# Optimization experiments

Hardware: AMD Instinct MI355X
Metric: run time of the kernel (lower is better)

Reference implementation:

```python
import jax, jax.numpy as jnp
import numpy as np

B, T, C = 1, 2048, 1024
H = 16
HD = C // H
BLOCK = 2048
NEG = float('-inf')

def setup_inputs() -> dict:
    key = jax.random.key(0)
    ks = jax.random.split(key, 6)
    x = jax.random.normal(ks[0], (B, T, C), dtype=jnp.float32)
    cumulative_scores = jax.random.normal(ks[1], (B, T), dtype=jnp.float32) * 0.1
    padding_mask = jnp.ones((B, T), dtype=jnp.float32)
    token_index = jax.random.randint(ks[2], (B, T), 0, BLOCK).astype(jnp.int64)
    w_attn = jax.random.normal(ks[3], (C, 3 * C), dtype=jnp.float32) * (1.0 / np.sqrt(C))
    b_attn = jnp.zeros((3 * C,), dtype=jnp.float32)
    w_proj = jax.random.normal(ks[4], (C, C), dtype=jnp.float32) * (1.0 / np.sqrt(C))
    b_proj = jnp.zeros((C,), dtype=jnp.float32)
    return dict(x=x, cumulative_scores=cumulative_scores, padding_mask=padding_mask,
                token_index=token_index, w_attn=w_attn, b_attn=b_attn,
                w_proj=w_proj, b_proj=b_proj)

def _rotate_half(z):
    z1, z2 = z[..., : z.shape[-1] // 2], z[..., z.shape[-1] // 2 :]
    return jnp.concatenate((-z2, z1), axis=-1)

def reference(x, cumulative_scores, padding_mask, token_index, w_attn, b_attn, w_proj, b_proj):
    # fused QKV projection
    qkv = x @ w_attn + b_attn                      # (B,T,3C)
    q, k, v = jnp.split(qkv, 3, axis=2)
    q = q.reshape(B, T, H, HD).transpose(0, 2, 1, 3)  # (B,H,T,HD)
    k = k.reshape(B, T, H, HD).transpose(0, 2, 1, 3)
    v = v.reshape(B, T, H, HD).transpose(0, 2, 1, 3)

    # dynamic per-token RoPE positions: global token counts (original scatter
    # broadcasts indices over batch, so counts are global across all batches)
    cnt = jnp.zeros((BLOCK,), jnp.float32).at[token_index.reshape(-1)].add(1.0)
    per_tok = (1.0 / (cnt + 1e-10))[token_index]       # (B,T)
    partial = jnp.cumsum(per_tok, axis=-1)             # (B,T) fractional positions

    inv_freq = 1.0 / (10000.0 ** (jnp.arange(0, HD, 2, dtype=jnp.float32) / HD))
    freqs = partial[..., None] * inv_freq              # (B,T,HD/2)
    emb = jnp.concatenate((freqs, freqs), axis=-1)     # (B,T,HD)
    cos = jnp.cos(emb)[:, None]                        # (B,1,T,HD)
    sin = jnp.sin(emb)[:, None]
    q = q * cos + _rotate_half(q) * sin
    k = k * cos + _rotate_half(k) * sin

    # 'fork' plan: overwrite last channel
    q = q.at[..., -1].set(1.0)
    k = k.at[..., -1].set(jnp.broadcast_to(cumulative_scores[:, None, :], (B, H, T)))

    # additive causal + padding mask (B,T,T)
    causal = jnp.where(jnp.tril(jnp.ones((T, T), jnp.bool_)), 0.0, NEG)
    pm = jnp.take_along_axis(padding_mask, token_index, axis=1)     # (B,T)
    outer = pm[:, :, None] * pm[:, None, :]
    pad_add = jnp.where(outer.astype(jnp.bool_), 0.0, NEG)
    mask = causal[None, :, :] + pad_add                              # (B,T,T)

    # scale v by exp(cumulative_scores)
    v = v * jnp.exp(cumulative_scores)[:, None, :, None]

    scores = jnp.einsum('bhqd,bhkd->bhqk', q, k) / np.sqrt(HD) + mask[:, None]
    probs = jax.nn.softmax(scores, axis=-1)
    y = jnp.einsum('bhqk,bhkd->bhqd', probs, v)        # (B,H,T,HD)
    y = y.transpose(0, 2, 1, 3).reshape(B, T, C)
    return y @ w_proj + b_proj
```

## Files before the change

kernel.cpp:

```cpp
#include <hip/hip_runtime.h>
#include <math.h>

#define T 2048
#define C 1024
#define H 16
#define HD 64
#define N3 (3*C)
#define NBLOCK 2048

typedef __attribute__((ext_vector_type(8))) short bf16x8;
typedef __attribute__((ext_vector_type(4))) float f32x4;

#define MFMA16(a, b, c) __builtin_amdgcn_mfma_f32_16x16x32_bf16((a), (b), (c), 0, 0, 0)

__device__ inline short f2bf(float f) {
    unsigned u; __builtin_memcpy(&u, &f, 4);
    unsigned r = (u + 0x7fffu + ((u >> 16) & 1u)) >> 16;
    return (short)r;
}
__device__ inline float bf2f(short s) {
    unsigned u = ((unsigned)(unsigned short)s) << 16;
    float f; __builtin_memcpy(&f, &u, 4);
    return f;
}

__device__ inline void gload_lds16(const void* g, void* l) {
    __builtin_amdgcn_global_load_lds((const __attribute__((address_space(1))) unsigned int*)g,
                                     (__attribute__((address_space(3))) unsigned int*)l,
                                     16, 0, 0);
}

__global__ __launch_bounds__(256) void pre_kernel(const float* __restrict__ x,
                                                  const float* __restrict__ w_attn,
                                                  const float* __restrict__ w_proj,
                                                  const int* __restrict__ tok,
                                                  const float* __restrict__ padmask,
                                                  short* __restrict__ xb,
                                                  short* __restrict__ wabT,
                                                  short* __restrict__ wpbT,
                                                  float* __restrict__ partial,
                                                  float* __restrict__ pm_tok) {
    int bid = blockIdx.x;
    int tid = threadIdx.x;
    if (bid == 3072) {
        __shared__ float cntS[NBLOCK];
        __shared__ float sums[256];
        #pragma unroll
        for (int j = 0; j < 8; ++j) cntS[tid * 8 + j] = 0.0f;
        __syncthreads();
        int tk[8];
        #pragma unroll
        for (int j = 0; j < 8; ++j) {
            tk[j] = tok[tid * 8 + j];
            atomicAdd(&cntS[tk[j]], 1.0f);
        }
        __syncthreads();
        float vals[8];
        float s = 0.0f;
        #pragma unroll
        for (int j = 0; j < 8; ++j) {
            s += 1.0f / (cntS[tk[j]] + 1e-10f);
            vals[j] = s;
            pm_tok[tid * 8 + j] = padmask[tk[j]];
        }
        sums[tid] = s;
        __syncthreads();
        for (int off = 1; off < 256; off <<= 1) {
            float v = (tid >= off) ? sums[tid - off] : 0.0f;
            __syncthreads();
            sums[tid] += v;
            __syncthreads();
        }
        float offset = (tid > 0) ? sums[tid - 1] : 0.0f;
        #pragma unroll
        for (int j = 0; j < 8; ++j) partial[tid * 8 + j] = offset + vals[j];
        return;
    }
    if (bid < 2048) {
        int i = bid * 1024 + tid * 4;
        float4 v = *(const float4*)(x + i);
        short4 o;
        o.x = f2bf(v.x); o.y = f2bf(v.y); o.z = f2bf(v.z); o.w = f2bf(v.w);
        *(short4*)(xb + i) = o;
        return;
    }
    __shared__ float S[64][65];
    const float* in; short* out; int Kd, Nd, bx, by;
    if (bid < 2816) {
        int b = bid - 2048;
        bx = b % 48; by = b / 48;
        in = w_attn; out = wabT; Kd = C; Nd = N3;
    } else {
        int b = bid - 2816;
        bx = b % 16; by = b / 16;
        in = w_proj; out = wpbT; Kd = C; Nd = C;
    }
    int n0 = bx * 64, k0 = by * 64;
    #pragma unroll
    for (int i = 0; i < 16; ++i) {
        int lin = tid + i * 256;
        int r = lin >> 6, c = lin & 63;
        S[r][c] = in[(size_t)(k0 + r) * Nd + n0 + c];
    }
    __syncthreads();
    #pragma unroll
    for (int i = 0; i < 16; ++i) {
        int lin = tid + i * 256;
        int rn = lin >> 6, ck = lin & 63;
        out[(size_t)(n0 + rn) * Kd + k0 + ck] = f2bf(S[ck][rn]);
    }
}

template <int OUT_BF16, int BNF>
__global__ __launch_bounds__(256) void gemm_bt(const short* __restrict__ A,
                                               const short* __restrict__ Bt,
                                               const float* __restrict__ bias,
                                               void* __restrict__ Cout,
                                               int M, int N, int K) {
    constexpr int BN = BNF * 32;
    __shared__ alignas(16) short As[128 * 32];
    __shared__ alignas(16) short Bs[BN * 32];
    int tid = threadIdx.x;
    int m0 = blockIdx.y * 128, n0 = blockIdx.x * BN;
    int w = tid >> 6, l = tid & 63;
    int wm = (w >> 1) * 64, wn = (w & 1) * (BNF * 16);
    int lq = l & 15, g = l >> 4;
    int prow = l >> 2, pcol = (l & 3) * 8;
    f32x4 acc[4][BNF] = {};
    for (int k0 = 0; k0 < K; k0 += 32) {
        #pragma unroll
        for (int i = 0; i < 2; ++i) {
            int c = w * 2 + i;
            int row = c * 16 + prow;
            gload_lds16(A + (size_t)(m0 + row) * K + k0 + pcol, As + c * 512);
        }
        #pragma unroll
        for (int i = 0; i < BNF / 2; ++i) {
            int c = w * (BNF / 2) + i;
            int row = c * 16 + prow;
            gload_lds16(Bt + (size_t)(n0 + row) * K + k0 + pcol, Bs + c * 512);
        }
        __syncthreads();
        bf16x8 af[4], bfr[BNF];
        #pragma unroll
        for (int f = 0; f < 4; ++f)
            af[f] = *(const bf16x8*)(As + (wm + f * 16 + lq) * 32 + g * 8);
        #pragma unroll
        for (int j = 0; j < BNF; ++j)
            bfr[j] = *(const bf16x8*)(Bs + (wn + j * 16 + lq) * 32 + g * 8);
        #pragma unroll
        for (int fi = 0; fi < 4; ++fi)
            #pragma unroll
            for (int fj = 0; fj < BNF; ++fj)
                acc[fi][fj] = MFMA16(af[fi], bfr[fj], acc[fi][fj]);
        __syncthreads();
    }
    #pragma unroll
    for (int fi = 0; fi < 4; ++fi)
        #pragma unroll
        for (int fj = 0; fj < BNF; ++fj)
            #pragma unroll
            for (int r = 0; r < 4; ++r) {
                int m = m0 + wm + fi * 16 + g * 4 + r;
                int n = n0 + wn + fj * 16 + lq;
                float v = acc[fi][fj][r] + bias[n];
                if (OUT_BF16) ((short*)Cout)[(size_t)m * N + n] = f2bf(v);
                else          ((float*)Cout)[(size_t)m * N + n] = v;
            }
}

__global__ __launch_bounds__(256) void ropevt(short* __restrict__ qkvb,
                                              const float* __restrict__ partial,
                                              const float* __restrict__ cumsc,
                                              const float* __restrict__ pm_tok,
                                              short* __restrict__ vbT) {
    __shared__ alignas(16) short S[64][72];
    __shared__ float efs[64];
    int bid = blockIdx.x;
    int tid = threadIdx.x;
    if (bid < 512) {
        int tg = tid >> 6, l = tid & 63;
        int t = bid * 4 + tg;
        int j = l & 31;
        float inv = exp2f(-(float)j * (13.287712379549449f / 32.0f));
        float ang = partial[t] * inv;
        float cs_own = cosf(ang), sn_own = sinf(ang);
        float csc = cumsc[t];
        float pmv = pm_tok[t];
        float qfix = (pmv != 0.0f) ? 1.0f : 0.0f;
        float kfix = (pmv != 0.0f) ? csc : -1e20f;

        int h = l >> 2, jb = (l & 3) * 8;
        short* row = qkvb + (size_t)t * N3;
        int c1 = h * 64 + jb;
        bf16x8 qlo = *(const bf16x8*)(row + c1);
        bf16x8 qhi = *(const bf16x8*)(row + c1 + 32);
        bf16x8 klo = *(const bf16x8*)(row + C + c1);
        bf16x8 khi = *(const bf16x8*)(row + C + c1 + 32);
        bf16x8 qlo2, qhi2, klo2, khi2;
        #pragma unroll
        for (int i = 0; i < 8; ++i) {
            float cs = __shfl(cs_own, jb + i);
            float sn = __shfl(sn_own, jb + i);
            float q1 = bf2f(qlo[i]), q2 = bf2f(qhi[i]);
            float k1 = bf2f(klo[i]), k2 = bf2f(khi[i]);
            float q2n = q2 * cs + q1 * sn;
            float k2n = k2 * cs + k1 * sn;
            if (jb + i == 31) { q2n = qfix; k2n = kfix; }
            qlo2[i] = f2bf(q1 * cs - q2 * sn);
            qhi2[i] = f2bf(q2n);
            klo2[i] = f2bf(k1 * cs - k2 * sn);
            khi2[i] = f2bf(k2n);
        }
        *(bf16x8*)(row + c1) = qlo2;
        *(bf16x8*)(row + c1 + 32) = qhi2;
        *(bf16x8*)(row + C + c1) = klo2;
        *(bf16x8*)(row + C + c1 + 32) = khi2;
        return;
    }
    int b = bid - 512;
    int h = b >> 5;
    int t0 = (b & 31) * 64;
    if (tid < 64) efs[tid] = __expf(cumsc[t0 + tid]);
    __syncthreads();
    #pragma unroll
    for (int e = 0; e < 2; ++e) {
        int s = tid * 2 + e;
        int r = s >> 3, c8 = (s & 7) * 8;
        bf16x8 v = *(const bf16x8*)(qkvb + (size_t)(t0 + r) * N3 + 2 * C + h * 64 + c8);
        float ef = efs[r];
        bf16x8 o;
        #pragma unroll
        for (int i = 0; i < 8; ++i) o[i] = f2bf(bf2f(v[i]) * ef);
        *(bf16x8*)&S[r][c8] = o;
    }
    __syncthreads();
    #pragma unroll
    for (int e = 0; e < 2; ++e) {
        int s = tid * 2 + e;
        int d = s >> 3, t8 = (s & 7) * 8;
        bf16x8 o;
        #pragma unroll
        for (int i = 0; i < 8; ++i) o[i] = S[t8 + i][d];
        *(bf16x8*)(vbT + (size_t)(h * 64 + d) * T + t0 + t8) = o;
    }
}

__global__ __launch_bounds__(256) void attn_flash(const short* __restrict__ qkvb,
                                                  const short* __restrict__ vbT,
                                                  short* __restrict__ yb) {
    __shared__ alignas(16) short Kt[2][64 * 64];
    __shared__ alignas(16) short Vt[2][64 * 64];
    __shared__ alignas(16) short Ps[4][16][72];

    int b = blockIdx.x;
    int h, qt;
    if (b < 256) { h = b & 15; qt = 31 - (b >> 4); }
    else         { int c2 = b - 256; h = c2 & 15; qt = c2 >> 4; }
    int tid = threadIdx.x;
    int w = tid >> 6, l = tid & 63;
    int lq = l & 15, g = l >> 4;
    int qrl = w * 16 + lq;

    const short* qbase = qkvb + (size_t)(qt * 64 + qrl) * N3 + h * 64;
    bf16x8 qf0 = *(const bf16x8*)(qbase + g * 8);
    bf16x8 qf1 = *(const bf16x8*)(qbase + 32 + g * 8);

    f32x4 accO[4] = {};
    float lsum = 0.0f;

    int srow = tid >> 3, scol = (tid & 7) * 8;
    const short* kgb = qkvb + C + h * 64 + scol;
    const short* vgb = vbT + (size_t)(h * 64) * T + scol;
    int wb0 = srow * 128 + ((scol * 2) ^ ((srow & 7) << 4));
    int wb1 = (srow + 32) * 128 + ((scol * 2) ^ ((srow & 7) << 4));

    auto do_tile = [&](int cur, bool masked) {
        const char* Kc = (const char*)Kt[cur];
        const char* Vc = (const char*)Vt[cur];
        f32x4 s[4] = {};
        #pragma unroll
        for (int f = 0; f < 4; ++f) {
            int row = f * 16 + lq;
            const char* kr_ = Kc + row * 128;
            int sw = (row & 7) << 4;
            bf16x8 a0 = *(const bf16x8*)(kr_ + ((g * 16) ^ sw));
            bf16x8 a1 = *(const bf16x8*)(kr_ + ((64 + g * 16) ^ sw));
            s[f] = MFMA16(a0, qf0, s[f]);
            s[f] = MFMA16(a1, qf1, s[f]);
        }
        float p[16];
        #pragma unroll
        for (int f = 0; f < 4; ++f)
            #pragma unroll
            for (int r = 0; r < 4; ++r) {
                float sv = s[f][r] * 0.125f;
                if (masked) {
                    int kl = f * 16 + g * 4 + r;
                    sv = (kl > qrl) ? -INFINITY : sv;
                }
                float pv = __expf(sv);
                p[f * 4 + r] = pv;
                lsum += pv;
            }
        #pragma unroll
        for (int f = 0; f < 4; ++f) {
            unsigned u0, u1;
            asm("v_cvt_pk_bf16_f32 %0, %1, %2" : "=v"(u0) : "v"(p[f * 4 + 0]), "v"(p[f * 4 + 1]));
            asm("v_cvt_pk_bf16_f32 %0, %1, %2" : "=v"(u1) : "v"(p[f * 4 + 2]), "v"(p[f * 4 + 3]));
            uint2 uu; uu.x = u0; uu.y = u1;
            *(uint2*)&Ps[w][lq][f * 16 + g * 4] = uu;
        }
        #pragma unroll
        for (int kh = 0; kh < 2; ++kh) {
            bf16x8 pa = *(const bf16x8*)&Ps[w][lq][kh * 32 + g * 8];
            #pragma unroll
            for (int f = 0; f < 4; ++f) {
                int vrow = f * 16 + lq;
                const char* vr_ = Vc + vrow * 128;
                bf16x8 vb = *(const bf16x8*)(vr_ + (((kh * 32 + g * 8) * 2) ^ ((vrow & 7) << 4)));
                accO[f] = MFMA16(pa, vb, accO[f]);
            }
        }
    };

    uint4 kr0 = *(const uint4*)(kgb + (size_t)srow * N3);
    uint4 kr1 = *(const uint4*)(kgb + (size_t)(srow + 32) * N3);
    uint4 vr0 = *(const uint4*)(vgb + (size_t)srow * T);
    uint4 vr1 = *(const uint4*)(vgb + (size_t)(srow + 32) * T);
    *(uint4*)((char*)Kt[0] + wb0) = kr0;
    *(uint4*)((char*)Kt[0] + wb1) = kr1;
    *(uint4*)((char*)Vt[0] + wb0) = vr0;
    *(uint4*)((char*)Vt[0] + wb1) = vr1;
    __syncthreads();

    for (int t = 0; t < qt; ++t) {
        int kn = (t + 1) * 64;
        kr0 = *(const uint4*)(kgb + (size_t)(kn + srow) * N3);
        kr1 = *(const uint4*)(kgb + (size_t)(kn + srow + 32) * N3);
        vr0 = *(const uint4*)(vgb + (size_t)srow * T + kn);
        vr1 = *(const uint4*)(vgb + (size_t)(srow + 32) * T + kn);

        do_tile(t & 1, false);

        int nxt = (t & 1) ^ 1;
        *(uint4*)((char*)Kt[nxt] + wb0) = kr0;
        *(uint4*)((char*)Kt[nxt] + wb1) = kr1;
        *(uint4*)((char*)Vt[nxt] + wb0) = vr0;
        *(uint4*)((char*)Vt[nxt] + wb1) = vr1;
        __syncthreads();
    }
    do_tile(qt & 1, true);

    lsum += __shfl_xor(lsum, 16);
    lsum += __shfl_xor(lsum, 32);
    float linv_own = 1.0f / lsum;
    float li[4];
    #pragma unroll
    for (int r = 0; r < 4; ++r) li[r] = __shfl(linv_own, g * 4 + r);

    #pragma unroll
    for (int f = 0; f < 4; ++f)
        #pragma unroll
        for (int r = 0; r < 4; ++r) {
            int trow = qt * 64 + w * 16 + g * 4 + r;
            yb[(size_t)trow * C + h * 64 + f * 16 + lq] = f2bf(accO[f][r] * li[r]);
        }
}

extern "C" void kernel_launch(void* const* d_in, const int* in_sizes, int n_in,
                              void* d_out, int out_size, void* d_ws, size_t ws_size,
                              hipStream_t stream) {
    const float* x       = (const float*)d_in[0];
    const float* cumsc   = (const float*)d_in[1];
    const float* padmask = (const float*)d_in[2];
    const int*   tok     = (const int*)d_in[3];
    const float* w_attn  = (const float*)d_in[4];
    const float* b_attn  = (const float*)d_in[5];
    const float* w_proj  = (const float*)d_in[6];
    const float* b_proj  = (const float*)d_in[7];
    float* out = (float*)d_out;

    float* part   = (float*)d_ws;
    float* pm_tok = part + 2048;
    short* xb     = (short*)(pm_tok + 2048);
    short* wabT   = xb + (size_t)T * C;
    short* wpbT   = wabT + (size_t)N3 * C;
    short* qkvb   = wpbT + (size_t)C * C;
    short* vbT    = qkvb + (size_t)T * N3;
    short* yb     = vbT + (size_t)C * T;

    pre_kernel<<<3073, 256, 0, stream>>>(x, w_attn, w_proj, tok, padmask,
                                         xb, wabT, wpbT, part, pm_tok);
    gemm_bt<1, 4><<<dim3(N3 / 128, T / 128), 256, 0, stream>>>(xb, wabT, b_attn, qkvb, T, N3, C);
    ropevt<<<1024, 256, 0, stream>>>(qkvb, part, cumsc, pm_tok, vbT);
    attn_flash<<<512, 256, 0, stream>>>(qkvb, vbT, yb);
    gemm_bt<0, 2><<<dim3(C / 64, T / 128), 256, 0, stream>>>(yb, wpbT, b_proj, out, T, C, C);
}
```

Baseline: 90.80 us.

## Double-buffer GEMM LDS tiles and raise wave priority around MFMA blocks

The bf16 GEMM now uses two LDS buffers: it issues the global-to-LDS loads for the next K slice before running MFMAs on the current one, with a single explicit vmcnt wait and barrier per iteration in place of two syncthreads. This aims to hide global load latency behind matrix math. s_setprio hints are also placed around the MFMA sections in both the GEMM and the attention tile loop so that waves in their compute phase get issue priority. The cost is doubled LDS per block, which may reduce occupancy.

```diff
diff --git a/kernel.cpp b/kernel.cpp
--- a/kernel.cpp
+++ b/kernel.cpp
@@ -118,8 +118,8 @@
                                                void* __restrict__ Cout,
                                                int M, int N, int K) {
     constexpr int BN = BNF * 32;
-    __shared__ alignas(16) short As[128 * 32];
-    __shared__ alignas(16) short Bs[BN * 32];
+    __shared__ alignas(16) short As[2][128 * 32];
+    __shared__ alignas(16) short Bs[2][BN * 32];
     int tid = threadIdx.x;
     int m0 = blockIdx.y * 128, n0 = blockIdx.x * BN;
     int w = tid >> 6, l = tid & 63;
@@ -127,34 +127,52 @@
     int lq = l & 15, g = l >> 4;
     int prow = l >> 2, pcol = (l & 3) * 8;
     f32x4 acc[4][BNF] = {};
-    for (int k0 = 0; k0 < K; k0 += 32) {
+
+    auto stage = [&](int buf, int k0) {
         #pragma unroll
         for (int i = 0; i < 2; ++i) {
             int c = w * 2 + i;
             int row = c * 16 + prow;
-            gload_lds16(A + (size_t)(m0 + row) * K + k0 + pcol, As + c * 512);
+            gload_lds16(A + (size_t)(m0 + row) * K + k0 + pcol, As[buf] + c * 512);
         }
         #pragma unroll
         for (int i = 0; i < BNF / 2; ++i) {
             int c = w * (BNF / 2) + i;
             int row = c * 16 + prow;
-            gload_lds16(Bt + (size_t)(n0 + row) * K + k0 + pcol, Bs + c * 512);
-        }
-        __syncthreads();
+            gload_lds16(Bt + (size_t)(n0 + row) * K + k0 + pcol, Bs[buf] + c * 512);
+        }
+    };
+
+    int NK = K / 32;
+    stage(0, 0);
+    asm volatile("s_waitcnt vmcnt(0)" ::: "memory");
+    __builtin_amdgcn_s_barrier();
+    __builtin_amdgcn_sched_barrier(0);
+
+    for (int t = 0; t < NK; ++t) {
+        int cur = t & 1;
+        if (t + 1 < NK) stage(cur ^ 1, (t + 1) * 32);
+
         bf16x8 af[4], bfr[BNF];
         #pragma unroll
         for (int f = 0; f < 4; ++f)
-            af[f] = *(const bf16x8*)(As + (wm + f * 16 + lq) * 32 + g * 8);
+            af[f] = *(const bf16x8*)(As[cur] + (wm + f * 16 + lq) * 32 + g * 8);
         #pragma unroll
         for (int j = 0; j < BNF; ++j)
-            bfr[j] = *(const bf16x8*)(Bs + (wn + j * 16 + lq) * 32 + g * 8);
+            bfr[j] = *(const bf16x8*)(Bs[cur] + (wn + j * 16 + lq) * 32 + g * 8);
+        __builtin_amdgcn_s_setprio(1);
         #pragma unroll
         for (int fi = 0; fi < 4; ++fi)
             #pragma unroll
             for (int fj = 0; fj < BNF; ++fj)
                 acc[fi][fj] = MFMA16(af[fi], bfr[fj], acc[fi][fj]);
-        __syncthreads();
-    }
+        __builtin_amdgcn_s_setprio(0);
+
+        asm volatile("s_waitcnt vmcnt(0)" ::: "memory");
+        __builtin_amdgcn_s_barrier();
+        __builtin_amdgcn_sched_barrier(0);
+    }
+
     #pragma unroll
     for (int fi = 0; fi < 4; ++fi)
         #pragma unroll
@@ -279,6 +297,7 @@
         const char* Kc = (const char*)Kt[cur];
         const char* Vc = (const char*)Vt[cur];
         f32x4 s[4] = {};
+        __builtin_amdgcn_s_setprio(1);
         #pragma unroll
         for (int f = 0; f < 4; ++f) {
             int row = f * 16 + lq;
@@ -289,6 +308,7 @@
             s[f] = MFMA16(a0, qf0, s[f]);
             s[f] = MFMA16(a1, qf1, s[f]);
         }
+        __builtin_amdgcn_s_setprio(0);
         float p[16];
         #pragma unroll
         for (int f = 0; f < 4; ++f)
@@ -311,6 +331,7 @@
             uint2 uu; uu.x = u0; uu.y = u1;
             *(uint2*)&Ps[w][lq][f * 16 + g * 4] = uu;
         }
+        __builtin_amdgcn_s_setprio(1);
         #pragma unroll
         for (int kh = 0; kh < 2; ++kh) {
             bf16x8 pa = *(const bf16x8*)&Ps[w][lq][kh * 32 + g * 8];
@@ -322,6 +343,7 @@
                 accO[f] = MFMA16(pa, vb, accO[f]);
             }
         }
+        __builtin_amdgcn_s_setprio(0);
     };
 
     uint4 kr0 = *(const uint4*)(kgb + (size_t)srow * N3);
```

Result: no change. 91.46 us (+0.7%).
